# Optimization experiments

Hardware: AMD Instinct MI355X
Metric: run time of the kernel (lower is better)

The kernel has to match this reference:

```python
import jax, jax.numpy as jnp
import numpy as np

NULL_IDX = 0  # word_to_idx['<NULL>']
N, T, D, WV, H, V = 128, 65, 512, 128, 128, 10000


def setup_inputs() -> dict:
    key = jax.random.key(0)
    ks = jax.random.split(key, 12)
    scale = 0.02
    return {
        "features": jax.random.normal(ks[0], (N, D), dtype=jnp.float32),
        "captions": jax.random.randint(ks[1], (N, T), 0, V, dtype=jnp.int32),
        # TemporalAffine(input_dim, hidden_dim)
        "W_proj": jax.random.normal(ks[2], (D, H), dtype=jnp.float32) * scale,
        "b_proj": jnp.zeros((H,), dtype=jnp.float32),
        # nn.Embedding(vocab_size, wordvec_dim)
        "embed": jax.random.normal(ks[3], (V, WV), dtype=jnp.float32) * scale,
        # nn.RNN(wordvec_dim, hidden_dim, num_layers=1) weights
        "W_ih": jax.random.normal(ks[4], (H, WV), dtype=jnp.float32) * scale,
        "W_hh": jax.random.normal(ks[5], (H, H), dtype=jnp.float32) * scale,
        "b_ih": jnp.zeros((H,), dtype=jnp.float32),
        "b_hh": jnp.zeros((H,), dtype=jnp.float32),
        # TemporalAffine(hidden_dim, vocab_size)
        "W_vocab": jax.random.normal(ks[6], (H, V), dtype=jnp.float32) * scale,
        "b_vocab": jnp.zeros((V,), dtype=jnp.float32),
    }


def reference(features, captions, W_proj, b_proj, embed, W_ih, W_hh, b_ih, b_hh, W_vocab, b_vocab):
    captions_in = captions[:, :-1]   # (N, T-1)
    captions_out = captions[:, 1:]   # (N, T-1)
    mask = (captions_out != NULL_IDX).astype(jnp.float32)

    # initial hidden state: affine projection of image features (no tanh)
    h0 = features @ W_proj + b_proj                      # (N, H)

    # word embeddings, time-major for scan
    x = embed[captions_in]                               # (N, T-1, WV)
    x_tm = jnp.swapaxes(x, 0, 1)                          # (T-1, N, WV)

    def step(h_prev, x_t):
        # vanilla RNN cell: tanh(x W_ih^T + b_ih + h W_hh^T + b_hh)
        h_new = jnp.tanh(x_t @ W_ih.T + b_ih + h_prev @ W_hh.T + b_hh)
        return h_new, h_new

    _, hs = jax.lax.scan(step, h0, x_tm)                  # (T-1, N, H)
    h = jnp.swapaxes(hs, 0, 1)                            # (N, T-1, H)

    # temporal affine to vocab scores
    scores = h @ W_vocab + b_vocab                        # (N, T-1, V)

    # temporal softmax loss, masked, averaged over batch size N
    logp = jax.nn.log_softmax(scores, axis=-1)
    nll = -jnp.take_along_axis(logp, captions_out[..., None], axis=-1)[..., 0]
    loss = jnp.sum(nll * mask) / captions.shape[0]
    return loss
```

## Files before the change

### kernel.cpp

```cpp
#include <hip/hip_runtime.h>
#include <hip/hip_bf16.h>
#include <math.h>

typedef __attribute__((ext_vector_type(8))) short short8;
typedef __attribute__((ext_vector_type(4))) float f32x4;
typedef __attribute__((ext_vector_type(4))) unsigned int u32x4;

#define NB   128
#define TT   64
#define DD   512
#define HH   128
#define WVD  128
#define VV   10000
#define VP   10048
#define NROW (NB*TT)
#define NTILE (VP/64)
#define VT   32
#define TILE_BYTES 16384
#define LOG2E 1.44269504088896f
#define LN2   0.69314718055995f

__device__ __forceinline__ unsigned short f2bf(float x) {
  union { float f; unsigned int u; } v; v.f = x;
  unsigned int r = v.u + 0x7fffu + ((v.u >> 16) & 1u);
  return (unsigned short)(r >> 16);
}
__device__ __forceinline__ float bf2f(unsigned short u) {
  union { unsigned int i; float f; } v; v.i = ((unsigned int)u) << 16; return v.f;
}
__device__ __forceinline__ short8 cvt2bf8(f32x4 a, f32x4 b) {
  short8 t;
  t[0]=(short)f2bf(a[0]); t[1]=(short)f2bf(a[1]);
  t[2]=(short)f2bf(a[2]); t[3]=(short)f2bf(a[3]);
  t[4]=(short)f2bf(b[0]); t[5]=(short)f2bf(b[1]);
  t[6]=(short)f2bf(b[2]); t[7]=(short)f2bf(b[3]);
  return t;
}

__global__ __launch_bounds__(256) void k_pre(
    const float* __restrict__ Wv, unsigned short* __restrict__ Wvt,
    const float* __restrict__ bv, float* __restrict__ expbv,
    float* __restrict__ out,
    const float* __restrict__ features, const float* __restrict__ Wp,
    const float* __restrict__ bp, float* __restrict__ h0,
    const int* __restrict__ captions, const float* __restrict__ embed,
    const float* __restrict__ Wih, const float* __restrict__ bih,
    const float* __restrict__ bhh, float* __restrict__ xbt) {
  __shared__ __align__(16) char smem[32768];
  int b = blockIdx.x, tid = threadIdx.x;

  if (b < 314) {
    float (*tile)[65] = (float (*)[65])smem;
    int bvv = (b >> 1) * 64;
    int bk  = (b & 1) * 64;
    int tv = tid & 63;
    int tk0 = tid >> 6;
    #pragma unroll
    for (int kk = 0; kk < 64; kk += 4) {
      int k = bk + kk + tk0;
      int v = bvv + tv;
      tile[kk + tk0][tv] = (v < VV) ? Wv[(size_t)k*VV + v] : 0.f;
    }
    __syncthreads();
    int tk = tid & 63;
    int tv0 = tid >> 6;
    #pragma unroll
    for (int vv = 0; vv < 64; vv += 4) {
      int v = bvv + vv + tv0;
      Wvt[(size_t)v*HH + bk + tk] = f2bf(tile[tk][vv + tv0] * LOG2E);
    }
  } else if (b < 354) {
    int v = (b - 314)*256 + tid;
    if (v < VP) expbv[v] = (v < VV) ? __expf(bv[v]) : 0.f;
  } else if (b == 354) {
    if (tid == 0) out[0] = 0.f;
  } else if (b < 483) {
    int n = b - 355;
    float* fl  = (float*)smem;
    f32x4* red = (f32x4*)(smem + 2048);
    fl[tid]       = features[n*DD + tid];
    fl[tid + 256] = features[n*DD + 256 + tid];
    __syncthreads();
    int jq = (tid & 31) * 4;
    int ks = tid >> 5;
    f32x4 acc = {0.f,0.f,0.f,0.f};
    const float* wp = Wp + (size_t)(ks*64)*HH + jq;
    #pragma unroll 4
    for (int k = 0; k < 64; ++k) {
      f32x4 wv = *(const f32x4*)(wp + (size_t)k*HH);
      acc += fl[ks*64 + k] * wv;
    }
    red[ks*32 + (tid & 31)] = acc;
    __syncthreads();
    if (tid < 32) {
      f32x4 s = red[tid];
      #pragma unroll
      for (int i = 1; i < 8; ++i) s += red[i*32 + tid];
      s += *(const f32x4*)(bp + tid*4);
      *(f32x4*)(h0 + n*HH + tid*4) = s;
    }
  } else {
    char* wihbf = smem;
    int w = tid >> 6, l = tid & 63;
    int l4 = l >> 4, lc = l & 15;
    {
      int row = tid >> 1, half = tid & 1;
      const float* src = Wih + (size_t)row*WVD + half*64;
      #pragma unroll
      for (int i = 0; i < 8; ++i) {
        f32x4 a = *(const f32x4*)(src + i*8);
        f32x4 c = *(const f32x4*)(src + i*8 + 4);
        int chunk = half*8 + i;
        *(short8*)(wihbf + row*256 + ((chunk << 4) ^ ((row & 7) << 4))) = cvt2bf8(a, c);
      }
    }
    int wrow = (b - 483)*256 + w*64;
    short8 af[4][4];
    #pragma unroll
    for (int sm = 0; sm < 4; ++sm) {
      int r = wrow + sm*16 + lc;
      int n = r >> 6, t = r & 63;
      const float* x = embed + (size_t)captions[n*65 + t] * WVD;
      #pragma unroll
      for (int ks = 0; ks < 4; ++ks) {
        const float* p = x + ks*32 + l4*8;
        af[sm][ks] = cvt2bf8(*(const f32x4*)p, *(const f32x4*)(p+4));
      }
    }
    __syncthreads();
    #pragma unroll
    for (int ct = 0; ct < 8; ++ct) {
      int rowb = ct*16 + lc;
      short8 bf[4];
      #pragma unroll
      for (int ks = 0; ks < 4; ++ks)
        bf[ks] = *(const short8*)(wihbf + rowb*256 + (((ks*4 + l4) << 4) ^ ((rowb & 7) << 4)));
      int col = ct*16 + lc;
      float bb = bih[col] + bhh[col];
      #pragma unroll
      for (int sm = 0; sm < 4; ++sm) {
        f32x4 acc = {0.f,0.f,0.f,0.f};
        #pragma unroll
        for (int ks = 0; ks < 4; ++ks)
          acc = __builtin_amdgcn_mfma_f32_16x16x32_bf16(af[sm][ks], bf[ks], acc, 0, 0, 0);
        #pragma unroll
        for (int jj = 0; jj < 4; ++jj)
          xbt[(size_t)(wrow + sm*16 + l4*4 + jj)*HH + col] = acc[jj] + bb;
      }
    }
  }
}

__global__ __launch_bounds__(256) void k_rnn(
    const float* __restrict__ h0, const float* __restrict__ xbt,
    const float* __restrict__ Whh, unsigned short* __restrict__ hsb) {
  __shared__ __align__(16) char smem[8192];
  int b = blockIdx.x, tid = threadIdx.x;
  int n0 = b * 16;
  int w = tid >> 6, l = tid & 63;
  int l4 = l >> 4, lc = l & 15;

  short8 bw[2][4];
  int jcol[2];
  #pragma unroll
  for (int c = 0; c < 2; ++c) {
    int jc = (2*w + c)*16 + lc;
    jcol[c] = jc;
    #pragma unroll
    for (int ks = 0; ks < 4; ++ks) {
      const float* p = Whh + (size_t)jc*HH + ks*32 + l4*8;
      bw[c][ks] = cvt2bf8(*(const f32x4*)p, *(const f32x4*)(p+4));
    }
  }

  {
    int s = tid >> 4, ch = tid & 15;
    const float* p = h0 + (size_t)(n0 + s)*HH + ch*8;
    f32x4 a = *(const f32x4*)p;
    f32x4 c = *(const f32x4*)(p + 4);
    *(short8*)(smem + s*256 + ((ch*16) ^ ((s&7)<<4))) = cvt2bf8(a, c);
  }

#define XLOAD(dst, t_) do {                                                   \
    if ((t_) < TT) {                                                          \
      _Pragma("unroll")                                                       \
      for (int c = 0; c < 2; ++c) {                                           \
        _Pragma("unroll")                                                     \
        for (int jj = 0; jj < 4; ++jj) {                                      \
          int s_ = l4*4 + jj;                                                 \
          dst[c][jj] = xbt[((size_t)(n0 + s_)*TT + (t_))*HH + jcol[c]];       \
        }                                                                     \
      }                                                                       \
    }                                                                         \
  } while (0)

  f32x4 x0[2], x1[2], x2[2];
  XLOAD(x0, 0); XLOAD(x1, 1); XLOAD(x2, 2);
  __syncthreads();

  int fs = tid >> 4;
  int fo = (tid & 15) * 16;
  int frd = fo ^ ((fs & 7) << 4);

  int cur = 0;
  for (int t = 0; t < TT; ++t) {
    short8 ah[4];
    #pragma unroll
    for (int ks = 0; ks < 4; ++ks)
      ah[ks] = *(const short8*)(smem + cur*4096 + lc*256 +
                                ((ks*64 + l4*16) ^ ((lc&7)<<4)));
    f32x4 acc[2] = {{0.f,0.f,0.f,0.f},{0.f,0.f,0.f,0.f}};
    #pragma unroll
    for (int ks = 0; ks < 4; ++ks) {
      acc[0] = __builtin_amdgcn_mfma_f32_16x16x32_bf16(ah[ks], bw[0][ks], acc[0], 0,0,0);
      acc[1] = __builtin_amdgcn_mfma_f32_16x16x32_bf16(ah[ks], bw[1][ks], acc[1], 0,0,0);
    }
    #pragma unroll
    for (int c = 0; c < 2; ++c) {
      #pragma unroll
      for (int jj = 0; jj < 4; ++jj) {
        int s = l4*4 + jj;
        float v = acc[c][jj] + x0[c][jj];
        float e = __builtin_amdgcn_exp2f(v * (2.0f*LOG2E));
        float h = 1.0f - 2.0f*__builtin_amdgcn_rcpf(e + 1.0f);
        *(unsigned short*)(smem + (cur^1)*4096 + s*256 +
                           ((jcol[c]*2) ^ ((s&7)<<4))) = f2bf(h);
      }
    }
    x0[0]=x1[0]; x0[1]=x1[1];
    x1[0]=x2[0]; x1[1]=x2[1];
    XLOAD(x2, t+3);
    __syncthreads();
    u32x4 fr = *(const u32x4*)(smem + (cur^1)*4096 + fs*256 + frd);
    *(u32x4*)(hsb + ((size_t)(n0 + fs)*TT + t)*HH + (fo >> 1)) = fr;
    cur ^= 1;
  }
#undef XLOAD
}

__global__ __launch_bounds__(256) void k_loss(
    const unsigned short* __restrict__ hsb,
    const unsigned short* __restrict__ wvt,
    const float* __restrict__ expbv,
    float* __restrict__ se_part) {
  __shared__ unsigned short bt[2][TILE_BYTES/2];
  int tid = threadIdx.x;
  int w = tid >> 6, l = tid & 63;
  int l4 = l >> 4, lc = l & 15;
  int rb = blockIdx.x >> 5;
  int vt = blockIdx.x & 31;
  int wrow = rb*256 + w*64;

  short8 af[4][4];
  #pragma unroll
  for (int sm = 0; sm < 4; ++sm)
    #pragma unroll
    for (int ks = 0; ks < 4; ++ks)
      af[sm][ks] = *(const short8*)(hsb + (size_t)(wrow + sm*16 + lc)*HH + ks*32 + l4*8);

  int T = (lc & 7) << 4;
  int sb[4];
  #pragma unroll
  for (int ks = 0; ks < 4; ++ks) sb[ks] = ((ks*64) + l4*16) ^ T;

#define STAGE(bufi, ct) do {                                                  \
    const char* _gb = (const char*)wvt + (size_t)(ct)*TILE_BYTES;             \
    _Pragma("unroll")                                                         \
    for (int q = 0; q < 4; ++q) {                                             \
      int _off = w*4096 + q*1024 + l*16;                                      \
      int _src = _off ^ (((_off >> 8) & 7) << 4);                             \
      __builtin_amdgcn_global_load_lds(                                       \
        (const __attribute__((address_space(1))) void*)(_gb + _src),          \
        (__attribute__((address_space(3))) void*)((char*)&bt[bufi][0] + w*4096 + q*1024), \
        16, 0, 0);                                                            \
    }                                                                         \
  } while (0)

#define EBLOAD(dst, ct) do {                                                  \
    const float* _e = expbv + (ct)*64 + lc;                                   \
    dst[0] = _e[0]; dst[1] = _e[16]; dst[2] = _e[32]; dst[3] = _e[48];        \
  } while (0)

#define COMPUTE(bufi, ebv_) do {                                              \
    const char* _Bb = (const char*)&bt[bufi][0];                              \
    _Pragma("unroll")                                                         \
    for (int st = 0; st < 4; ++st) {                                          \
      const char* _Bs = _Bb + st*4096 + lc*256;                               \
      short8 _b0 = *(const short8*)(_Bs + sb[0]);                             \
      short8 _b1 = *(const short8*)(_Bs + sb[1]);                             \
      short8 _b2 = *(const short8*)(_Bs + sb[2]);                             \
      short8 _b3 = *(const short8*)(_Bs + sb[3]);                             \
      float _eb = ebv_[st];                                                   \
      _Pragma("unroll")                                                       \
      for (int sm = 0; sm < 4; ++sm) {                                        \
        f32x4 _acc = {0.f,0.f,0.f,0.f};                                       \
        _acc = __builtin_amdgcn_mfma_f32_16x16x32_bf16(af[sm][0], _b0, _acc, 0,0,0); \
        _acc = __builtin_amdgcn_mfma_f32_16x16x32_bf16(af[sm][1], _b1, _acc, 0,0,0); \
        _acc = __builtin_amdgcn_mfma_f32_16x16x32_bf16(af[sm][2], _b2, _acc, 0,0,0); \
        _acc = __builtin_amdgcn_mfma_f32_16x16x32_bf16(af[sm][3], _b3, _acc, 0,0,0); \
        _Pragma("unroll")                                                     \
        for (int jj = 0; jj < 4; ++jj)                                        \
          se[sm][jj] = fmaf(__builtin_amdgcn_exp2f(_acc[jj]), _eb, se[sm][jj]); \
      }                                                                       \
    }                                                                         \
  } while (0)

  float se[4][4] = {{0.f}};
  float ebc[4], ebn[4];
  STAGE(0, vt);
  EBLOAD(ebc, vt);
  __syncthreads();
  int i = 0;
  for (;;) {
    int nextct = vt + (i+1)*VT;
    if (nextct < NTILE) { STAGE((i+1)&1, nextct); EBLOAD(ebn, nextct); }
    COMPUTE(i&1, ebc);
    if (nextct >= NTILE) break;
    __syncthreads();
    ebc[0]=ebn[0]; ebc[1]=ebn[1]; ebc[2]=ebn[2]; ebc[3]=ebn[3];
    ++i;
  }

  #pragma unroll
  for (int sm = 0; sm < 4; ++sm)
    #pragma unroll
    for (int jj = 0; jj < 4; ++jj) {
      float v = se[sm][jj];
      v += __shfl_xor(v, 1); v += __shfl_xor(v, 2);
      v += __shfl_xor(v, 4); v += __shfl_xor(v, 8);
      se[sm][jj] = v;
    }
  if (lc == 0) {
    #pragma unroll
    for (int sm = 0; sm < 4; ++sm)
      #pragma unroll
      for (int jj = 0; jj < 4; ++jj)
        se_part[(size_t)vt*NROW + wrow + sm*16 + l4*4 + jj] = se[sm][jj];
  }
#undef STAGE
#undef EBLOAD
#undef COMPUTE
}

__global__ __launch_bounds__(256) void k_final(
    const unsigned short* __restrict__ hsb,
    const unsigned short* __restrict__ wvt,
    const float* __restrict__ bv,
    const float* __restrict__ se_part,
    const int* __restrict__ captions,
    float* __restrict__ out) {
  int tid = threadIdx.x;
  int w = tid >> 6, l = tid & 63;
  int row = blockIdx.x*32 + w*8 + (l >> 3);
  int seg = l & 7;
  int n = row >> 6, t = row & 63;
  int tg = captions[n*65 + t + 1];
  float sep = 0.f;
  #pragma unroll
  for (int i = 0; i < 4; ++i)
    sep += se_part[(size_t)(seg*4 + i)*NROW + row];
  float part = 0.f;
  if (tg != 0) {
    const unsigned short* a = hsb + (size_t)row*HH + seg*16;
    const unsigned short* bq = wvt + (size_t)tg*HH + seg*16;
    short8 a0 = *(const short8*)a, a1 = *(const short8*)(a+8);
    short8 b0 = *(const short8*)bq, b1 = *(const short8*)(bq+8);
    #pragma unroll
    for (int i = 0; i < 8; ++i) {
      part += bf2f((unsigned short)a0[i]) * bf2f((unsigned short)b0[i]);
      part += bf2f((unsigned short)a1[i]) * bf2f((unsigned short)b1[i]);
    }
  }
  part += __shfl_xor(part, 1); sep += __shfl_xor(sep, 1);
  part += __shfl_xor(part, 2); sep += __shfl_xor(sep, 2);
  part += __shfl_xor(part, 4); sep += __shfl_xor(sep, 4);
  if (seg == 0 && tg != 0) {
    float score = part * LN2 + bv[tg];
    float nll = logf(sep) - score;
    atomicAdd(out, nll * (1.0f/128.0f));
  }
}

extern "C" void kernel_launch(void* const* d_in, const int* in_sizes, int n_in,
                              void* d_out, int out_size, void* d_ws, size_t ws_size,
                              hipStream_t stream) {
  const float* features = (const float*)d_in[0];
  const int*   captions = (const int*)d_in[1];
  const float* W_proj   = (const float*)d_in[2];
  const float* b_proj   = (const float*)d_in[3];
  const float* embed    = (const float*)d_in[4];
  const float* W_ih     = (const float*)d_in[5];
  const float* W_hh     = (const float*)d_in[6];
  const float* b_ih     = (const float*)d_in[7];
  const float* b_hh     = (const float*)d_in[8];
  const float* W_vocab  = (const float*)d_in[9];
  const float* b_vocab  = (const float*)d_in[10];
  float* out = (float*)d_out;
  char* ws = (char*)d_ws;

  float*          h0      = (float*)(ws + 0x000000);
  float*          se_part = (float*)(ws + 0x010000);
  unsigned short* hsb     = (unsigned short*)(ws + 0x410000);
  unsigned short* wvt     = (unsigned short*)(ws + 0x620000);
  float*          expbv   = (float*)(ws + 0x8A0000);
  float*          xbt     = (float*)(ws + 0x8B0000);

  hipLaunchKernelGGL(k_pre, dim3(515), dim3(256), 0, stream,
                     W_vocab, wvt, b_vocab, expbv, out,
                     features, W_proj, b_proj, h0,
                     captions, embed, W_ih, b_ih, b_hh, xbt);
  hipLaunchKernelGGL(k_rnn, dim3(8), dim3(256), 0, stream,
                     h0, xbt, W_hh, hsb);
  hipLaunchKernelGGL(k_loss, dim3(32*VT), dim3(256), 0, stream,
                     hsb, wvt, expbv, se_part);
  hipLaunchKernelGGL(k_final, dim3(NROW/32), dim3(256), 0, stream,
                     hsb, wvt, b_vocab, se_part, captions, out);
}
```

Before: 108.2 us.

## Reorder xbt layout for coalesced RNN loads and streamline recurrence loop

The input projection xbt is now written by k_pre in a permuted layout matching the RNN's MFMA lane order, so each lane in k_rnn loads its per-step x values as two contiguous f32x4 vectors instead of eight scattered scalar loads. The recurrence loop is manually unrolled by two with precomputed LDS pointers, split accumulators for shorter MFMA dependency chains, a packed bf16 conversion instruction and a lighter barrier that waits only on LDS counters. These changes target latency on the serial 64-step critical path. They add inline assembly and rely on the sched_barrier-based ordering being correct.

```diff
diff --git a/kernel.cpp b/kernel.cpp
--- a/kernel.cpp
+++ b/kernel.cpp
@@ -35,6 +35,18 @@
   t[4]=(short)f2bf(b[0]); t[5]=(short)f2bf(b[1]);
   t[6]=(short)f2bf(b[2]); t[7]=(short)f2bf(b[3]);
   return t;
+}
+__device__ __forceinline__ unsigned int cvtpk(float lo, float hi) {
+  unsigned int r;
+  asm("v_cvt_pk_bf16_f32 %0, %1, %2" : "=v"(r) : "v"(lo), "v"(hi));
+  return r;
+}
+
+__device__ __forceinline__ void lds_barrier() {
+  asm volatile("s_waitcnt lgkmcnt(0)" ::: "memory");
+  __builtin_amdgcn_s_barrier();
+  asm volatile("" ::: "memory");
+  __builtin_amdgcn_sched_barrier(0);
 }
 
 __global__ __launch_bounds__(256) void k_pre(
@@ -114,13 +126,18 @@
         *(short8*)(wihbf + row*256 + ((chunk << 4) ^ ((row & 7) << 4))) = cvt2bf8(a, c);
       }
     }
-    int wrow = (b - 483)*256 + w*64;
+    int bp2 = b - 483;
+    int wrow = bp2*256 + w*64;
+    int nn = bp2*4 + w;
+    int g = nn >> 4;
+    int sr = nn & 15;
+    int l4r = sr >> 2, jjr = sr & 3;
+    int lanebase = (l4r*16 + lc)*4 + jjr;
     short8 af[4][4];
     #pragma unroll
     for (int sm = 0; sm < 4; ++sm) {
-      int r = wrow + sm*16 + lc;
-      int n = r >> 6, t = r & 63;
-      const float* x = embed + (size_t)captions[n*65 + t] * WVD;
+      int t = sm*16 + lc;
+      const float* x = embed + (size_t)captions[nn*65 + t] * WVD;
       #pragma unroll
       for (int ks = 0; ks < 4; ++ks) {
         const float* p = x + ks*32 + l4*8;
@@ -144,8 +161,10 @@
         for (int ks = 0; ks < 4; ++ks)
           acc = __builtin_amdgcn_mfma_f32_16x16x32_bf16(af[sm][ks], bf[ks], acc, 0, 0, 0);
         #pragma unroll
-        for (int jj = 0; jj < 4; ++jj)
-          xbt[(size_t)(wrow + sm*16 + l4*4 + jj)*HH + col] = acc[jj] + bb;
+        for (int jj = 0; jj < 4; ++jj) {
+          int t = sm*16 + l4*4 + jj;
+          xbt[(size_t)(g*512 + t*8 + ct)*256 + lanebase] = acc[jj] + bb;
+        }
       }
     }
   }
@@ -176,66 +195,92 @@
   {
     int s = tid >> 4, ch = tid & 15;
     const float* p = h0 + (size_t)(n0 + s)*HH + ch*8;
-    f32x4 a = *(const f32x4*)p;
-    f32x4 c = *(const f32x4*)(p + 4);
-    *(short8*)(smem + s*256 + ((ch*16) ^ ((s&7)<<4))) = cvt2bf8(a, c);
-  }
-
-#define XLOAD(dst, t_) do {                                                   \
-    if ((t_) < TT) {                                                          \
-      _Pragma("unroll")                                                       \
-      for (int c = 0; c < 2; ++c) {                                           \
-        _Pragma("unroll")                                                     \
-        for (int jj = 0; jj < 4; ++jj) {                                      \
-          int s_ = l4*4 + jj;                                                 \
-          dst[c][jj] = xbt[((size_t)(n0 + s_)*TT + (t_))*HH + jcol[c]];       \
-        }                                                                     \
-      }                                                                       \
+    *(short8*)(smem + s*256 + ((ch*16) ^ ((s&7)<<4))) =
+        cvt2bf8(*(const f32x4*)p, *(const f32x4*)(p + 4));
+  }
+
+  const char* rd0[4]; const char* rd1[4];
+  #pragma unroll
+  for (int ks = 0; ks < 4; ++ks) {
+    int off = lc*256 + ((ks*64 + l4*16) ^ ((lc&7)<<4));
+    rd0[ks] = smem + off;
+    rd1[ks] = smem + 4096 + off;
+  }
+  char* wr0[8]; char* wr1[8];
+  #pragma unroll
+  for (int c = 0; c < 2; ++c)
+    #pragma unroll
+    for (int jj = 0; jj < 4; ++jj) {
+      int s = l4*4 + jj;
+      int off = s*256 + ((jcol[c]*2) ^ ((s&7)<<4));
+      wr0[c*4+jj] = smem + 4096 + off;
+      wr1[c*4+jj] = smem + off;
+    }
+  int fs = tid >> 4, fo = (tid & 15) * 16;
+  const char* fr0 = smem + fs*256 + (fo ^ ((fs&7)<<4));
+  const char* fr1 = fr0 + 4096;
+  unsigned short* hst = hsb + (size_t)(n0 + fs)*TT*HH + (fo >> 1) - HH;
+
+  const float* xpE = xbt + ((size_t)b*512 + w*2)*256 + l*4;
+  const float* xpO = xpE + 2048;
+  f32x4 xA0 = *(const f32x4*)xpE, xA1 = *(const f32x4*)(xpE + 256);
+  xpE += 4096;
+  f32x4 xB0 = *(const f32x4*)xpO, xB1 = *(const f32x4*)(xpO + 256);
+  xpO += 4096;
+
+  lds_barrier();
+
+#define MFMA16(a,b_,c) __builtin_amdgcn_mfma_f32_16x16x32_bf16(a,b_,c,0,0,0)
+#define BODY(RD, FR, WR, X0, X1, XP, DOSTORE) do {                            \
+    short8 ah0 = *(const short8*)RD[0];                                       \
+    short8 ah1 = *(const short8*)RD[1];                                       \
+    short8 ah2 = *(const short8*)RD[2];                                       \
+    short8 ah3 = *(const short8*)RD[3];                                       \
+    f32x4 xn0 = *(const f32x4*)XP;                                            \
+    f32x4 xn1 = *(const f32x4*)(XP + 256);                                    \
+    XP += 4096;                                                               \
+    if (DOSTORE) { u32x4 fv = *(const u32x4*)FR; *(u32x4*)hst = fv; }         \
+    hst += HH;                                                                \
+    f32x4 aA0={0.f,0.f,0.f,0.f}, aA1={0.f,0.f,0.f,0.f};                       \
+    f32x4 aB0={0.f,0.f,0.f,0.f}, aB1={0.f,0.f,0.f,0.f};                       \
+    aA0 = MFMA16(ah0, bw[0][0], aA0); aA1 = MFMA16(ah0, bw[1][0], aA1);       \
+    aB0 = MFMA16(ah2, bw[0][2], aB0); aB1 = MFMA16(ah2, bw[1][2], aB1);       \
+    aA0 = MFMA16(ah1, bw[0][1], aA0); aA1 = MFMA16(ah1, bw[1][1], aA1);       \
+    aB0 = MFMA16(ah3, bw[0][3], aB0); aB1 = MFMA16(ah3, bw[1][3], aB1);       \
+    float hv0[4], hv1[4];                                                     \
+    _Pragma("unroll")                                                         \
+    for (int jj = 0; jj < 4; ++jj) {                                          \
+      float v0 = aA0[jj] + aB0[jj] + X0[jj];                                  \
+      float e0 = __builtin_amdgcn_exp2f(v0 * (2.0f*LOG2E));                   \
+      hv0[jj] = fmaf(-2.0f, __builtin_amdgcn_rcpf(e0 + 1.0f), 1.0f);          \
+      float v1 = aA1[jj] + aB1[jj] + X1[jj];                                  \
+      float e1 = __builtin_amdgcn_exp2f(v1 * (2.0f*LOG2E));                   \
+      hv1[jj] = fmaf(-2.0f, __builtin_amdgcn_rcpf(e1 + 1.0f), 1.0f);          \
     }                                                                         \
+    X0 = xn0; X1 = xn1;                                                       \
+    unsigned int p01 = cvtpk(hv0[0], hv0[1]), p23 = cvtpk(hv0[2], hv0[3]);    \
+    unsigned int q01 = cvtpk(hv1[0], hv1[1]), q23 = cvtpk(hv1[2], hv1[3]);    \
+    *(unsigned short*)WR[0] = (unsigned short)p01;                            \
+    *(unsigned short*)WR[1] = (unsigned short)(p01 >> 16);                    \
+    *(unsigned short*)WR[2] = (unsigned short)p23;                            \
+    *(unsigned short*)WR[3] = (unsigned short)(p23 >> 16);                    \
+    *(unsigned short*)WR[4] = (unsigned short)q01;                            \
+    *(unsigned short*)WR[5] = (unsigned short)(q01 >> 16);                    \
+    *(unsigned short*)WR[6] = (unsigned short)q23;                            \
+    *(unsigned short*)WR[7] = (unsigned short)(q23 >> 16);                    \
+    lds_barrier();                                                            \
   } while (0)
 
-  f32x4 x0[2], x1[2], x2[2];
-  XLOAD(x0, 0); XLOAD(x1, 1); XLOAD(x2, 2);
-  __syncthreads();
-
-  int fs = tid >> 4;
-  int fo = (tid & 15) * 16;
-  int frd = fo ^ ((fs & 7) << 4);
-
-  int cur = 0;
-  for (int t = 0; t < TT; ++t) {
-    short8 ah[4];
-    #pragma unroll
-    for (int ks = 0; ks < 4; ++ks)
-      ah[ks] = *(const short8*)(smem + cur*4096 + lc*256 +
-                                ((ks*64 + l4*16) ^ ((lc&7)<<4)));
-    f32x4 acc[2] = {{0.f,0.f,0.f,0.f},{0.f,0.f,0.f,0.f}};
-    #pragma unroll
-    for (int ks = 0; ks < 4; ++ks) {
-      acc[0] = __builtin_amdgcn_mfma_f32_16x16x32_bf16(ah[ks], bw[0][ks], acc[0], 0,0,0);
-      acc[1] = __builtin_amdgcn_mfma_f32_16x16x32_bf16(ah[ks], bw[1][ks], acc[1], 0,0,0);
-    }
-    #pragma unroll
-    for (int c = 0; c < 2; ++c) {
-      #pragma unroll
-      for (int jj = 0; jj < 4; ++jj) {
-        int s = l4*4 + jj;
-        float v = acc[c][jj] + x0[c][jj];
-        float e = __builtin_amdgcn_exp2f(v * (2.0f*LOG2E));
-        float h = 1.0f - 2.0f*__builtin_amdgcn_rcpf(e + 1.0f);
-        *(unsigned short*)(smem + (cur^1)*4096 + s*256 +
-                           ((jcol[c]*2) ^ ((s&7)<<4))) = f2bf(h);
-      }
-    }
-    x0[0]=x1[0]; x0[1]=x1[1];
-    x1[0]=x2[0]; x1[1]=x2[1];
-    XLOAD(x2, t+3);
-    __syncthreads();
-    u32x4 fr = *(const u32x4*)(smem + (cur^1)*4096 + fs*256 + frd);
-    *(u32x4*)(hsb + ((size_t)(n0 + fs)*TT + t)*HH + (fo >> 1)) = fr;
-    cur ^= 1;
-  }
-#undef XLOAD
+  BODY(rd0, fr0, wr0, xA0, xA1, xpE, 0);
+  BODY(rd1, fr1, wr1, xB0, xB1, xpO, 1);
+  #pragma unroll 1
+  for (int it = 1; it < 32; ++it) {
+    BODY(rd0, fr0, wr0, xA0, xA1, xpE, 1);
+    BODY(rd1, fr1, wr1, xB0, xB1, xpO, 1);
+  }
+  { u32x4 fv = *(const u32x4*)fr0; *(u32x4*)hst = fv; }
+#undef BODY
+#undef MFMA16
 }
 
 __global__ __launch_bounds__(256) void k_loss(
```

Result: faster. 96.33 us (-11.0%).
